# Performance work log

Measured on AMD Instinct MI355X. Metric: run time of the kernel, lower is better.

The kernel has to match this reference:

```python
import jax, jax.numpy as jnp
import numpy as np
import math

N_HEAD = 16
N_KV_HEAD = 4
N_EMBED = 2048
HEAD_DIM = N_EMBED // N_HEAD  # 128
ROPE_BASE = 10000.0


def _rope_tables(T, dim, dtype):
    inv_freq = 1.0 / (ROPE_BASE ** (jnp.arange(0, dim, 2, dtype=jnp.float32) / dim))
    t = jnp.arange(T, dtype=jnp.float32)
    freqs = jnp.outer(t, inv_freq)            # (T, dim/2)
    emb = jnp.concatenate([freqs, freqs], -1) # (T, dim)
    return jnp.cos(emb).astype(dtype), jnp.sin(emb).astype(dtype)


def _rotate_half(x):
    half = x.shape[-1] // 2
    return jnp.concatenate([-x[..., half:], x[..., :half]], axis=-1)


def setup_inputs() -> dict:
    key = jax.random.key(0)
    kx, kq, kk, kv, ko = jax.random.split(key, 5)
    B, T, C = 2, 2048, N_EMBED
    s = 0.02
    return {
        "x": jax.random.normal(kx, (B, T, C), jnp.float32),
        "Wq": jax.random.normal(kq, (N_HEAD * HEAD_DIM, C), jnp.float32) * s,
        "Wk": jax.random.normal(kk, (N_KV_HEAD * HEAD_DIM, C), jnp.float32) * s,
        "Wv": jax.random.normal(kv, (N_KV_HEAD * HEAD_DIM, C), jnp.float32) * s,
        "Wo": jax.random.normal(ko, (C, N_HEAD * HEAD_DIM), jnp.float32) * s,
    }


def reference(x, Wq, Wk, Wv, Wo):
    B, T, C = x.shape
    H, KV, D = N_HEAD, N_KV_HEAD, HEAD_DIM
    rep = H // KV

    q = jnp.einsum('btc,oc->bto', x, Wq).reshape(B, T, H, D).transpose(0, 2, 1, 3)   # (B,H,T,D)
    k = jnp.einsum('btc,oc->bto', x, Wk).reshape(B, T, KV, D).transpose(0, 2, 1, 3)  # (B,KV,T,D)
    v = jnp.einsum('btc,oc->bto', x, Wv).reshape(B, T, KV, D).transpose(0, 2, 1, 3)

    cos, sin = _rope_tables(T, D, x.dtype)  # (T,D) broadcast over (B,h,T,D)
    q = q * cos + _rotate_half(q) * sin
    k = k * cos + _rotate_half(k) * sin

    # GQA: head h attends to kv head h // rep (== repeat_interleave in torch).
    qg = q.reshape(B, KV, rep, T, D)
    scale = 1.0 / math.sqrt(D)
    attn = jnp.einsum('bgrtd,bgsd->bgrts', qg, k) * scale  # (B,KV,rep,T,T)
    causal = jnp.tril(jnp.ones((T, T), dtype=bool))
    attn = jnp.where(causal, attn, -jnp.inf)
    attn = jax.nn.softmax(attn, axis=-1)
    out = jnp.einsum('bgrts,bgsd->bgrtd', attn, v)          # (B,KV,rep,T,D)
    out = out.reshape(B, H, T, D).transpose(0, 2, 1, 3).reshape(B, T, H * D)
    return jnp.einsum('bto,co->btc', out, Wo)
```

## Files before the change

kernel.cpp:

```cpp
#include <hip/hip_runtime.h>
#include <stdint.h>

typedef unsigned short u16;
typedef __attribute__((ext_vector_type(8))) short short8;
typedef __attribute__((ext_vector_type(4))) short short4v;
typedef __attribute__((ext_vector_type(4))) float f32x4;

#define NB_  2
#define NT_  2048
#define NC_  2048
#define NH_  16
#define NKV_ 4
#define HD_  128
#define NM_  (NB_*NT_)
#define NQKV 3072

__device__ __forceinline__ u16 f2b(float x) {
  uint32_t u = __float_as_uint(x);
  u += 0x7fffu + ((u >> 16) & 1u);
  return (u16)(u >> 16);
}
__device__ __forceinline__ float b2f(u16 x) {
  return __uint_as_float(((uint32_t)x) << 16);
}
__device__ __forceinline__ uint32_t pk2t(float a, float b) {
  return (__float_as_uint(a) >> 16) | (__float_as_uint(b) & 0xFFFF0000u);
}

typedef __attribute__((address_space(1))) uint32_t* gp1_t;
typedef __attribute__((address_space(3))) uint32_t* lp3_t;
__device__ __forceinline__ void async_ld16(const void* g, void* l) {
  __builtin_amdgcn_global_load_lds((gp1_t)(uintptr_t)g, (lp3_t)(uintptr_t)l, 16, 0, 0);
}

__global__ void f2bf_all(const float* __restrict__ x,  const float* __restrict__ wq,
                         const float* __restrict__ wk, const float* __restrict__ wv,
                         const float* __restrict__ wo,
                         u16* xb, u16* wqb, u16* wkb, u16* wvb, u16* wob) {
  int bid = blockIdx.x;
  const float* src; u16* dst; int base;
  if      (bid < 8192)  { src = x;  dst = xb;  base = bid; }
  else if (bid < 12288) { src = wq; dst = wqb; base = bid - 8192; }
  else if (bid < 13312) { src = wk; dst = wkb; base = bid - 12288; }
  else if (bid < 14336) { src = wv; dst = wvb; base = bid - 13312; }
  else                  { src = wo; dst = wob; base = bid - 14336; }
  int i = base * 256 + threadIdx.x;
  const float4 v = ((const float4*)src)[i];
  short4v o;
  o[0] = (short)f2b(v.x); o[1] = (short)f2b(v.y);
  o[2] = (short)f2b(v.z); o[3] = (short)f2b(v.w);
  *(short4v*)(dst + (size_t)i * 4) = o;
}

__global__ void postk(const u16* __restrict__ qkv,
                      u16* __restrict__ Qr, u16* __restrict__ Kr, u16* __restrict__ Vt) {
  __shared__ u16 tile[64][72];
  int bid = blockIdx.x;
  if (bid < 20480) {
    u16* out; int nheads; int tid; int coff; float osc;
    if (bid < 16384) { out = Qr; nheads = NH_;  tid = bid * 256 + threadIdx.x; coff = 0;
                       osc = 0.08838834764831845f; }
    else             { out = Kr; nheads = NKV_; tid = (bid - 16384) * 256 + threadIdx.x; coff = 2048;
                       osc = 1.0f; }
    int j = tid & 63;
    int t = (tid >> 6) & (NT_ - 1);
    int bh = tid >> 17;
    int h = bh % nheads, b = bh / nheads;
    const u16* src = qkv + ((size_t)(b * NT_ + t)) * NQKV + coff + h * HD_;
    float q0 = b2f(src[j]), q1 = b2f(src[j + 64]);
    float inv = expf(-0.14391156831212787f * (float)j);
    float ang = (float)t * inv;
    float c = cosf(ang), s = sinf(ang);
    u16* dst = out + ((size_t)(b * nheads + h) * NT_ + t) * HD_;
    dst[j]      = f2b((q0 * c - q1 * s) * osc);
    dst[j + 64] = f2b((q1 * c + q0 * s) * osc);
  } else {
    int idx = bid - 20480;
    int tt = idx & 63, dd = idx >> 6;
    int tid = threadIdx.x;
    int r = tid >> 3, c8 = (tid & 7) * 8;
#pragma unroll
    for (int it = 0; it < 2; ++it) {
      int row = r + it * 32;
      short8 v = *(const short8*)(qkv + (size_t)(tt * 64 + row) * NQKV + 2560 + dd * 64 + c8);
      *(short8*)(&tile[row][c8]) = v;
    }
    __syncthreads();
    int b = (tt * 64) >> 11, t0 = (tt * 64) & (NT_ - 1);
    int dl = tid >> 3, t8 = (tid & 7) * 8;
#pragma unroll
    for (int it = 0; it < 2; ++it) {
      int d = dl + it * 32;
      int gcol = dd * 64 + d;
      int kv = gcol >> 7, drow = gcol & 127;
      short8 v;
#pragma unroll
      for (int k = 0; k < 8; ++k) v[k] = (short)tile[t8 + k][d];
      *(short8*)(Vt + ((size_t)(b * NKV_ + kv) * HD_ + drow) * NT_ + t0 + t8) = v;
    }
  }
}

__global__ __launch_bounds__(256, 2)
void gemm192(const u16* __restrict__ A, const u16* __restrict__ B, u16* __restrict__ C, int K)
{
  __shared__ u16 As[2 * 128 * 32];
  __shared__ u16 Bs[2 * 192 * 32];
  const int bx = blockIdx.x, by = blockIdx.y;
  const int m0 = by * 128, n0 = bx * 192;
  const int tid = threadIdx.x;
  const int wave = tid >> 6, lane = tid & 63;
  const int quad = lane >> 4, l15 = lane & 15;
  const int wm = wave >> 1, wn = wave & 1;

  const int p_local = lane >> 3;
  const int s7 = lane & 7;
  const int mlo = s7 >> 2;
  const int gg = (s7 & 3) ^ (p_local & 3);
  const int rowc = p_local * 2 + mlo;
  const int kel = gg * 8;

  const u16* Ag[2]; u16* Al[2];
#pragma unroll
  for (int q = 0; q < 2; ++q) {
    const int c = wave * 2 + q;
    Ag[q] = A + (size_t)(m0 + c * 16 + rowc) * K + kel;
    Al[q] = As + c * 512;
  }
  const u16* Bg[3]; u16* Bl[3];
#pragma unroll
  for (int q = 0; q < 3; ++q) {
    const int c = wave * 3 + q;
    Bg[q] = B + (size_t)(n0 + c * 16 + rowc) * K + kel;
    Bl[q] = Bs + c * 512;
  }

  f32x4 acc[4][6] = {};

  int a_addr[4], b_addr[6];
#pragma unroll
  for (int i = 0; i < 4; ++i) {
    int m = wm * 64 + i * 16 + l15;
    a_addr[i] = ((m >> 1) * 8 + (m & 1) * 4 + (quad ^ ((m >> 1) & 3))) * 8;
  }
#pragma unroll
  for (int i = 0; i < 6; ++i) {
    int n = wn * 96 + i * 16 + l15;
    b_addr[i] = ((n >> 1) * 8 + (n & 1) * 4 + (quad ^ ((n >> 1) & 3))) * 8;
  }

  const int nk = K >> 5;
#pragma unroll
  for (int q = 0; q < 2; ++q) async_ld16(Ag[q], Al[q]);
#pragma unroll
  for (int q = 0; q < 3; ++q) async_ld16(Bg[q], Bl[q]);

  for (int i = 0; i < nk; ++i) {
    __syncthreads();
    if (i + 1 < nk) {
      const int offA = ((i + 1) & 1) * 4096;
      const int offB = ((i + 1) & 1) * 6144;
      const int k0 = (i + 1) << 5;
#pragma unroll
      for (int q = 0; q < 2; ++q) async_ld16(Ag[q] + k0, Al[q] + offA);
#pragma unroll
      for (int q = 0; q < 3; ++q) async_ld16(Bg[q] + k0, Bl[q] + offB);
    }
    const int offA = (i & 1) * 4096;
    const int offB = (i & 1) * 6144;
    short8 af[4], bf[6];
#pragma unroll
    for (int j = 0; j < 4; ++j) af[j] = *(const short8*)(As + offA + a_addr[j]);
#pragma unroll
    for (int j = 0; j < 6; ++j) bf[j] = *(const short8*)(Bs + offB + b_addr[j]);
#pragma unroll
    for (int mb = 0; mb < 4; ++mb)
#pragma unroll
      for (int nb = 0; nb < 6; ++nb)
        acc[mb][nb] = __builtin_amdgcn_mfma_f32_16x16x32_bf16(af[mb], bf[nb], acc[mb][nb], 0, 0, 0);
  }

#pragma unroll
  for (int mb = 0; mb < 4; ++mb)
#pragma unroll
    for (int nb = 0; nb < 6; ++nb) {
      const int gn = n0 + wn * 96 + nb * 16 + l15;
#pragma unroll
      for (int r = 0; r < 4; ++r) {
        const int gm = m0 + wm * 64 + mb * 16 + quad * 4 + r;
        C[(size_t)gm * NQKV + gn] = f2b(acc[mb][nb][r]);
      }
    }
}

__global__ __launch_bounds__(256, 2)
void gemm128o(const u16* __restrict__ A, const u16* __restrict__ B, float* __restrict__ C, int K)
{
  __shared__ u16 As[2 * 128 * 32];
  __shared__ u16 Bs[2 * 128 * 32];
  const int bx = blockIdx.x, by = blockIdx.y;
  const int m0 = by * 128, n0 = bx * 128;
  const int tid = threadIdx.x;
  const int wave = tid >> 6, lane = tid & 63;
  const int quad = lane >> 4, l15 = lane & 15;
  const int wm = wave >> 1, wn = wave & 1;

  const int p_local = lane >> 3;
  const int s7 = lane & 7;
  const int mlo = s7 >> 2;
  const int gg = (s7 & 3) ^ (p_local & 3);
  const int rowc = p_local * 2 + mlo;
  const int kel = gg * 8;

  const u16* Ag[2]; const u16* Bg[2];
  u16* Al[2]; u16* Bl[2];
#pragma unroll
  for (int q = 0; q < 2; ++q) {
    const int c = wave * 2 + q;
    Ag[q] = A + (size_t)(m0 + c * 16 + rowc) * K + kel;
    Bg[q] = B + (size_t)(n0 + c * 16 + rowc) * K + kel;
    Al[q] = As + c * 512;
    Bl[q] = Bs + c * 512;
  }

  f32x4 acc[4][4] = {};

  int a_addr[4], b_addr[4];
#pragma unroll
  for (int i = 0; i < 4; ++i) {
    int m = wm * 64 + i * 16 + l15;
    a_addr[i] = ((m >> 1) * 8 + (m & 1) * 4 + (quad ^ ((m >> 1) & 3))) * 8;
    int n = wn * 64 + i * 16 + l15;
    b_addr[i] = ((n >> 1) * 8 + (n & 1) * 4 + (quad ^ ((n >> 1) & 3))) * 8;
  }

  const int nk = K >> 5;
#pragma unroll
  for (int q = 0; q < 2; ++q) {
    async_ld16(Ag[q], Al[q]);
    async_ld16(Bg[q], Bl[q]);
  }

  for (int i = 0; i < nk; ++i) {
    __syncthreads();
    if (i + 1 < nk) {
      const int off = ((i + 1) & 1) * 4096;
      const int k0 = (i + 1) << 5;
#pragma unroll
      for (int q = 0; q < 2; ++q) {
        async_ld16(Ag[q] + k0, Al[q] + off);
        async_ld16(Bg[q] + k0, Bl[q] + off);
      }
    }
    const int off = (i & 1) * 4096;
    short8 af[4], bf[4];
#pragma unroll
    for (int j = 0; j < 4; ++j) af[j] = *(const short8*)(As + off + a_addr[j]);
#pragma unroll
    for (int j = 0; j < 4; ++j) bf[j] = *(const short8*)(Bs + off + b_addr[j]);
#pragma unroll
    for (int mb = 0; mb < 4; ++mb)
#pragma unroll
      for (int nb = 0; nb < 4; ++nb)
        acc[mb][nb] = __builtin_amdgcn_mfma_f32_16x16x32_bf16(af[mb], bf[nb], acc[mb][nb], 0, 0, 0);
  }

#pragma unroll
  for (int mb = 0; mb < 4; ++mb)
#pragma unroll
    for (int nb = 0; nb < 4; ++nb) {
      const int gn = n0 + wn * 64 + nb * 16 + l15;
#pragma unroll
      for (int r = 0; r < 4; ++r) {
        const int gm = m0 + wm * 64 + mb * 16 + quad * 4 + r;
        C[(size_t)gm * NC_ + gn] = acc[mb][nb][r];
      }
    }
}

__global__ __launch_bounds__(512, 4)
void attn_kernel(const u16* __restrict__ Q, const u16* __restrict__ Kg,
                 const u16* __restrict__ Vt, u16* __restrict__ O)
{
  __shared__ u16 Ks[2 * 8192];
  __shared__ u16 Vs[2 * 8192];
  const int bx = blockIdx.x;
  const int h  = blockIdx.y;
  const int b  = blockIdx.z;
  const int qi = b ? (15 - bx) : bx;
  const int kv = h >> 2;
  const int tid = threadIdx.x;
  const int wave = tid >> 6, lane = tid & 63;
  const int quad = lane >> 4, l15 = lane & 15;
  const int qw = qi * 128 + wave * 16;

  const u16* Kbase = Kg + (size_t)(b * NKV_ + kv) * NT_ * HD_;
  const u16* Vbase = Vt + (size_t)(b * NKV_ + kv) * HD_ * NT_;

  short8 qf[4];
  {
    const u16* qb = Q + ((size_t)(b * NH_ + h) * NT_ + qw + l15) * HD_ + quad * 8;
#pragma unroll
    for (int kb = 0; kb < 4; ++kb) qf[kb] = *(const short8*)(qb + kb * 32);
  }

  const int krow = lane >> 4, kgs = lane & 15;
  const int vrow = lane >> 3, vgs = lane & 7;

  auto stage = [&](int kt, int pbuf) {
    u16* KsB = Ks + pbuf * 8192;
    u16* VsB = Vs + pbuf * 8192;
#pragma unroll
    for (int qq = 0; qq < 2; ++qq) {
      const int c = wave * 2 + qq;
      const int rk = c * 4 + krow;
      const int gk = kgs ^ (rk & 7);
      async_ld16(Kbase + (size_t)(kt * 64 + rk) * HD_ + gk * 8, KsB + c * 512);
      const int rv = c * 8 + vrow;
      const int gv = vgs ^ (rv & 7);
      async_ld16(Vbase + (size_t)rv * NT_ + kt * 64 + gv * 8, VsB + c * 512);
    }
  };

  short8 vone;
#pragma unroll
  for (int j = 0; j < 8; ++j) vone[j] = (short)0x3F80;

  f32x4 acc_o[8] = {};
  f32x4 acc_l = {};
  const int nkt = 2 * qi + 2;

  stage(0, 0);

  for (int kt = 0; kt < nkt; ++kt) {
    __syncthreads();
    if (kt + 1 < nkt) stage(kt + 1, (kt + 1) & 1);
    if (kt * 64 > qw + 15) continue;

    const u16* KsB = Ks + (kt & 1) * 8192;
    const u16* VsB = Vs + (kt & 1) * 8192;

    f32x4 S[4] = {};
    __builtin_amdgcn_s_setprio(1);
#pragma unroll
    for (int nb = 0; nb < 4; ++nb) {
      const int row = nb * 16 + l15;
#pragma unroll
      for (int kb = 0; kb < 4; ++kb) {
        const int gi = kb * 4 + quad;
        short8 kfr = *(const short8*)(KsB + row * 128 + (gi ^ (row & 7)) * 8);
        S[nb] = __builtin_amdgcn_mfma_f32_16x16x32_bf16(kfr, qf[kb], S[nb], 0, 0, 0);
      }
    }
    __builtin_amdgcn_s_setprio(0);

    if (kt * 64 + 63 > qw) {
      const int qg = qw + l15;
#pragma unroll
      for (int nb = 0; nb < 4; ++nb)
#pragma unroll
        for (int r = 0; r < 4; ++r) {
          const int key = kt * 64 + nb * 16 + quad * 4 + r;
          if (key > qg) S[nb][r] = -INFINITY;
        }
    }

#pragma unroll
    for (int nb = 0; nb < 4; ++nb)
#pragma unroll
      for (int r = 0; r < 4; ++r)
        S[nb][r] = __expf(S[nb][r]);

    short8 pf[2];
    {
      uint32_t d0[4], d1[4];
#pragma unroll
      for (int nb = 0; nb < 4; ++nb) {
        d0[nb] = pk2t(S[nb][0], S[nb][1]);
        d1[nb] = pk2t(S[nb][2], S[nb][3]);
      }
      const int srcA = ((quad & 1) * 2) * 16 + l15;
      const int srcB = srcA + 16;
      const bool hi = quad >= 2;
#pragma unroll
      for (int k2 = 0; k2 < 2; ++k2) {
        const int nbL = k2 * 2, nbH = k2 * 2 + 1;
        uint32_t a0 = (uint32_t)__shfl((int)d0[nbL], srcA);
        uint32_t a1 = (uint32_t)__shfl((int)d1[nbL], srcA);
        uint32_t a2 = (uint32_t)__shfl((int)d0[nbL], srcB);
        uint32_t a3 = (uint32_t)__shfl((int)d1[nbL], srcB);
        uint32_t b0 = (uint32_t)__shfl((int)d0[nbH], srcA);
        uint32_t b1 = (uint32_t)__shfl((int)d1[nbH], srcA);
        uint32_t b2 = (uint32_t)__shfl((int)d0[nbH], srcB);
        uint32_t b3 = (uint32_t)__shfl((int)d1[nbH], srcB);
        uint32_t w[4] = { hi ? b0 : a0, hi ? b1 : a1, hi ? b2 : a2, hi ? b3 : a3 };
        pf[k2] = *(short8*)w;
      }
    }

    acc_l = __builtin_amdgcn_mfma_f32_16x16x32_bf16(pf[0], vone, acc_l, 0, 0, 0);
    acc_l = __builtin_amdgcn_mfma_f32_16x16x32_bf16(pf[1], vone, acc_l, 0, 0, 0);

    __builtin_amdgcn_s_setprio(1);
#pragma unroll
    for (int db = 0; db < 8; ++db) {
      const int row = db * 16 + l15;
#pragma unroll
      for (int k2 = 0; k2 < 2; ++k2) {
        const int gi = k2 * 4 + quad;
        short8 vf = *(const short8*)(VsB + row * 64 + (gi ^ (row & 7)) * 8);
        acc_o[db] = __builtin_amdgcn_mfma_f32_16x16x32_bf16(pf[k2], vf, acc_o[db], 0, 0, 0);
      }
    }
    __builtin_amdgcn_s_setprio(0);
  }

  {
    float inv_r[4];
#pragma unroll
    for (int r = 0; r < 4; ++r) inv_r[r] = 1.f / acc_l[r];
    const size_t orow = ((size_t)b * NT_ + qw) * (NH_ * HD_);
#pragma unroll
    for (int db = 0; db < 8; ++db)
#pragma unroll
      for (int r = 0; r < 4; ++r)
        O[orow + (size_t)(quad * 4 + r) * (NH_ * HD_) + h * HD_ + db * 16 + l15] =
            f2b(acc_o[db][r] * inv_r[r]);
  }
}

extern "C" void kernel_launch(void* const* d_in, const int* in_sizes, int n_in,
                              void* d_out, int out_size, void* d_ws, size_t ws_size,
                              hipStream_t stream) {
  const float* x  = (const float*)d_in[0];
  const float* Wq = (const float*)d_in[1];
  const float* Wk = (const float*)d_in[2];
  const float* Wv = (const float*)d_in[3];
  const float* Wo = (const float*)d_in[4];
  float* out = (float*)d_out;
  char* ws = (char*)d_ws;
  const size_t MB = (size_t)1 << 20;
  u16* xb    = (u16*)(ws + 0);
  u16* wqkv  = (u16*)(ws + 16 * MB);
  u16* wkb   = (u16*)(ws + 24 * MB);
  u16* wvb   = (u16*)(ws + 26 * MB);
  u16* wob   = (u16*)(ws + 28 * MB);
  u16* qkvrw = (u16*)(ws + 36 * MB);
  u16* Qr    = (u16*)(ws + 60 * MB);
  u16* Kr    = (u16*)(ws + 76 * MB);
  u16* Vtb   = (u16*)(ws + 80 * MB);
  u16* Ob    = xb;

  f2bf_all<<<18432, 256, 0, stream>>>(x, Wq, Wk, Wv, Wo, xb, wqkv, wkb, wvb, wob);

  gemm192<<<dim3(16, 32), 256, 0, stream>>>(xb, wqkv, qkvrw, 2048);

  postk<<<20992, 256, 0, stream>>>(qkvrw, Qr, Kr, Vtb);

  attn_kernel<<<dim3(16, 16, 2), 512, 0, stream>>>(Qr, Kr, Vtb, Ob);

  gemm128o<<<dim3(16, 32), 256, 0, stream>>>(Ob, wob, out, 2048);
}
```

Before: 285.9 us.

## Precompute RoPE cos/sin table and read K fragments directly from global memory

RoPE cos/sin values are now computed once into a table by extra blocks in the conversion kernel, so the post-processing kernel does a table lookup instead of expf/cosf/sinf per element. The attention kernel stops staging K tiles in LDS. Each wave loads its K MFMA fragments straight from global memory, which removes half the async LDS traffic and halves LDS use. The trade-off is that K reads are now redundant across the 8 waves and exposed to global latency, relying on L1/L2 hits instead.

```diff
diff --git a/kernel.cpp b/kernel.cpp
--- a/kernel.cpp
+++ b/kernel.cpp
@@ -36,8 +36,17 @@
 __global__ void f2bf_all(const float* __restrict__ x,  const float* __restrict__ wq,
                          const float* __restrict__ wk, const float* __restrict__ wv,
                          const float* __restrict__ wo,
-                         u16* xb, u16* wqb, u16* wkb, u16* wvb, u16* wob) {
+                         u16* xb, u16* wqb, u16* wkb, u16* wvb, u16* wob,
+                         float2* __restrict__ tab) {
   int bid = blockIdx.x;
+  if (bid >= 18432) {
+    int idx = (bid - 18432) * 256 + threadIdx.x;
+    int t = idx >> 6, j = idx & 63;
+    float inv = expf(-0.14391156831212787f * (float)j);
+    float ang = (float)t * inv;
+    tab[idx] = make_float2(cosf(ang), sinf(ang));
+    return;
+  }
   const float* src; u16* dst; int base;
   if      (bid < 8192)  { src = x;  dst = xb;  base = bid; }
   else if (bid < 12288) { src = wq; dst = wqb; base = bid - 8192; }
@@ -52,7 +61,7 @@
   *(short4v*)(dst + (size_t)i * 4) = o;
 }
 
-__global__ void postk(const u16* __restrict__ qkv,
+__global__ void postk(const u16* __restrict__ qkv, const float2* __restrict__ tab,
                       u16* __restrict__ Qr, u16* __restrict__ Kr, u16* __restrict__ Vt) {
   __shared__ u16 tile[64][72];
   int bid = blockIdx.x;
@@ -68,9 +77,8 @@
     int h = bh % nheads, b = bh / nheads;
     const u16* src = qkv + ((size_t)(b * NT_ + t)) * NQKV + coff + h * HD_;
     float q0 = b2f(src[j]), q1 = b2f(src[j + 64]);
-    float inv = expf(-0.14391156831212787f * (float)j);
-    float ang = (float)t * inv;
-    float c = cosf(ang), s = sinf(ang);
+    float2 cs = tab[t * 64 + j];
+    float c = cs.x, s = cs.y;
     u16* dst = out + ((size_t)(b * nheads + h) * NT_ + t) * HD_;
     dst[j]      = f2b((q0 * c - q1 * s) * osc);
     dst[j + 64] = f2b((q1 * c + q0 * s) * osc);
@@ -282,7 +290,6 @@
 void attn_kernel(const u16* __restrict__ Q, const u16* __restrict__ Kg,
                  const u16* __restrict__ Vt, u16* __restrict__ O)
 {
-  __shared__ u16 Ks[2 * 8192];
   __shared__ u16 Vs[2 * 8192];
   const int bx = blockIdx.x;
   const int h  = blockIdx.y;
@@ -304,23 +311,20 @@
     for (int kb = 0; kb < 4; ++kb) qf[kb] = *(const short8*)(qb + kb * 32);
   }
 
-  const int krow = lane >> 4, kgs = lane & 15;
   const int vrow = lane >> 3, vgs = lane & 7;
 
   auto stage = [&](int kt, int pbuf) {
-    u16* KsB = Ks + pbuf * 8192;
     u16* VsB = Vs + pbuf * 8192;
 #pragma unroll
     for (int qq = 0; qq < 2; ++qq) {
       const int c = wave * 2 + qq;
-      const int rk = c * 4 + krow;
-      const int gk = kgs ^ (rk & 7);
-      async_ld16(Kbase + (size_t)(kt * 64 + rk) * HD_ + gk * 8, KsB + c * 512);
       const int rv = c * 8 + vrow;
       const int gv = vgs ^ (rv & 7);
       async_ld16(Vbase + (size_t)rv * NT_ + kt * 64 + gv * 8, VsB + c * 512);
     }
   };
+
+  const u16* Kfrag = Kbase + (size_t)l15 * HD_ + quad * 8;
 
   short8 vone;
 #pragma unroll
@@ -337,20 +341,21 @@
     if (kt + 1 < nkt) stage(kt + 1, (kt + 1) & 1);
     if (kt * 64 > qw + 15) continue;
 
-    const u16* KsB = Ks + (kt & 1) * 8192;
     const u16* VsB = Vs + (kt & 1) * 8192;
 
     f32x4 S[4] = {};
     __builtin_amdgcn_s_setprio(1);
 #pragma unroll
     for (int nb = 0; nb < 4; ++nb) {
-      const int row = nb * 16 + l15;
-#pragma unroll
-      for (int kb = 0; kb < 4; ++kb) {
-        const int gi = kb * 4 + quad;
-        short8 kfr = *(const short8*)(KsB + row * 128 + (gi ^ (row & 7)) * 8);
-        S[nb] = __builtin_amdgcn_mfma_f32_16x16x32_bf16(kfr, qf[kb], S[nb], 0, 0, 0);
-      }
+      const u16* kr = Kfrag + (size_t)(kt * 64 + nb * 16) * HD_;
+      short8 kf0 = *(const short8*)(kr);
+      short8 kf1 = *(const short8*)(kr + 32);
+      short8 kf2 = *(const short8*)(kr + 64);
+      short8 kf3 = *(const short8*)(kr + 96);
+      S[nb] = __builtin_amdgcn_mfma_f32_16x16x32_bf16(kf0, qf[0], S[nb], 0, 0, 0);
+      S[nb] = __builtin_amdgcn_mfma_f32_16x16x32_bf16(kf1, qf[1], S[nb], 0, 0, 0);
+      S[nb] = __builtin_amdgcn_mfma_f32_16x16x32_bf16(kf2, qf[2], S[nb], 0, 0, 0);
+      S[nb] = __builtin_amdgcn_mfma_f32_16x16x32_bf16(kf3, qf[3], S[nb], 0, 0, 0);
     }
     __builtin_amdgcn_s_setprio(0);
 
@@ -449,13 +454,14 @@
   u16* Qr    = (u16*)(ws + 60 * MB);
   u16* Kr    = (u16*)(ws + 76 * MB);
   u16* Vtb   = (u16*)(ws + 80 * MB);
+  float2* tab = (float2*)(ws + 84 * MB);
   u16* Ob    = xb;
 
-  f2bf_all<<<18432, 256, 0, stream>>>(x, Wq, Wk, Wv, Wo, xb, wqkv, wkb, wvb, wob);
+  f2bf_all<<<18944, 256, 0, stream>>>(x, Wq, Wk, Wv, Wo, xb, wqkv, wkb, wvb, wob, tab);
 
   gemm192<<<dim3(16, 32), 256, 0, stream>>>(xb, wqkv, qkvrw, 2048);
 
-  postk<<<20992, 256, 0, stream>>>(qkvrw, Qr, Kr, Vtb);
+  postk<<<20992, 256, 0, stream>>>(qkvrw, tab, Qr, Kr, Vtb);
 
   attn_kernel<<<dim3(16, 16, 2), 512, 0, stream>>>(Qr, Kr, Vtb, Ob);
 
```

Measured after the change: 401.7 us. +40.5%, slower.
